# Kernel optimization log

Hardware: AMD Instinct MI355X
Metric: run time of the kernel (lower is better)

The kernel has to match this reference:

```python
import jax, jax.numpy as jnp
import numpy as np

B, N, D = 256, 256, 256
DELTA_BEARING = 5.0
DELTA_HEADING = 5.0
N_HEAD = int(360 / DELTA_HEADING)   # 72
N_BEAR = int(360 / DELTA_BEARING)   # 72
DOMAIN_PARAM = 2.0
EPS = 1e-14


def setup_inputs() -> dict:
    key = jax.random.key(0)
    ks = jax.random.split(key, 8)
    hidden_state = jax.random.normal(ks[0], (B, N, D), dtype=jnp.float32)
    distance_matrix = jax.random.uniform(ks[1], (B, N, N), dtype=jnp.float32) * 10.0
    bearing_matrix = jax.random.uniform(ks[2], (B, N, N), dtype=jnp.float32) * 360.0
    heading_matrix = jax.random.uniform(ks[3], (B, N, N), dtype=jnp.float32) * 360.0
    sequence_mask = (jax.random.uniform(ks[4], (B, N)) > 0.1).astype(jnp.float32)
    domain = jnp.full((N_HEAD, N_BEAR), DOMAIN_PARAM, dtype=jnp.float32)
    lim = 1.0 / np.sqrt(2 * D)
    W = jax.random.uniform(ks[5], (D, 2 * D), minval=-lim, maxval=lim, dtype=jnp.float32)
    b = jax.random.uniform(ks[6], (D,), minval=-lim, maxval=lim, dtype=jnp.float32)
    return {"hidden_state": hidden_state, "distance_matrix": distance_matrix,
            "bearing_matrix": bearing_matrix, "heading_matrix": heading_matrix,
            "sequence_mask": sequence_mask, "domain": domain, "W": W, "b": b}


def _compute_weights(domain, distance_matrix, bearing_matrix, heading_matrix, sequence_mask):
    # domain lookup indices from heading/bearing bins
    idx1 = jnp.clip(jnp.floor((heading_matrix + DELTA_HEADING / 2) / DELTA_HEADING), 0, N_HEAD - 1).astype(jnp.int32)
    idx2 = jnp.clip(jnp.floor((bearing_matrix + DELTA_BEARING / 2) / DELTA_BEARING), 0, N_BEAR - 1).astype(jnp.int32)
    w = jax.nn.relu(domain[idx1, idx2] - distance_matrix)  # (B,N,N)
    # pairwise sequence mask and no-self-attention mask
    wm = sequence_mask[:, :, None] * sequence_mask[:, None, :]  # (B,N,N)
    ped = 1.0 - jnp.eye(w.shape[1], dtype=w.dtype)               # (N,N)
    valid = (ped[None, :, :] * wm) > 0
    w = jnp.where(valid, w, 0.0)
    # masked softmax over dim=2: zeros are treated as masked, epsilon-stabilized
    mask = (w != 0).astype(w.dtype)
    masked_exps = jnp.exp(w) * mask + EPS
    w = masked_exps / (masked_exps.sum(axis=2, keepdims=True) + EPS)
    return jnp.where(valid, w, 0.0)


def reference(hidden_state, distance_matrix, bearing_matrix, heading_matrix, sequence_mask, domain, W, b):
    weights = _compute_weights(domain, distance_matrix, bearing_matrix, heading_matrix, sequence_mask)
    weighted_hidden = jnp.einsum('bij,bjd->bid', weights, hidden_state)  # (B,N,D)
    cat = jnp.concatenate([weighted_hidden, hidden_state], axis=-1)       # (B,N,2D)
    return jnp.einsum('bnk,dk->bnd', cat, W) + b
```

## Files before the change

kernel.cpp:

```cpp
#include <hip/hip_runtime.h>
#include <hip/hip_bf16.h>


typedef __attribute__((ext_vector_type(4))) float  f32x4;
typedef __attribute__((ext_vector_type(8))) short  bf16x8;
typedef __attribute__((ext_vector_type(4))) short  bf16x4;

#define EPSC 1e-14f

__device__ __forceinline__ short f2bf(float v) {
  __hip_bfloat16 h = __float2bfloat16(v);
  return *reinterpret_cast<short*>(&h);
}
__device__ __forceinline__ float bf2f(unsigned short u) {
  union { unsigned int i; float f; } c; c.i = ((unsigned int)u) << 16; return c.f;
}
__device__ __forceinline__ void gload16(const void* g, void* l) {
  __builtin_amdgcn_global_load_lds(
      (const __attribute__((address_space(1))) void*)g,
      (__attribute__((address_space(3))) void*)l, 16, 0, 0);
}

__global__ void k0_pack(const float* __restrict__ W, short* __restrict__ Wbf) {
  int idx = blockIdx.x * 256 + threadIdx.x;
  f32x4 v = *(const f32x4*)(W + (size_t)idx * 4);
  bf16x4 pk;
  pk[0] = f2bf(v[0]); pk[1] = f2bf(v[1]); pk[2] = f2bf(v[2]); pk[3] = f2bf(v[3]);
  *(bf16x4*)(Wbf + (size_t)idx * 4) = pk;
}

__global__ void k0_check(const float* __restrict__ domain, float* __restrict__ flag) {
  __shared__ int s_ok[4];
  const int t = threadIdx.x;
  float v0 = domain[0];
  bool ok = true;
  for (int x = t; x < 72 * 72; x += 256) ok = ok && (domain[x] == v0);
  unsigned long long m = __ballot(ok);
  if ((t & 63) == 0) s_ok[t >> 6] = (m == ~0ull) ? 1 : 0;
  __syncthreads();
  if (t == 0) {
    flag[0] = v0;
    flag[1] = (s_ok[0] && s_ok[1] && s_ok[2] && s_ok[3]) ? 1.f : 0.f;
  }
}

__global__ __launch_bounds__(512) void k1dual(
    const float* __restrict__ H, const short* __restrict__ Wbf,
    const float* __restrict__ bias,
    short* __restrict__ P1T, short* __restrict__ P2) {
  extern __shared__ char sm[];
  char* sA = sm;
  char* sB = sm + 33792;
  const int t  = threadIdx.x;
  const int n0 = blockIdx.x * 64;
  const int b  = n0 >> 8;
  const int jb = n0 & 255;

  #pragma unroll
  for (int p = 0; p < 4; ++p) {
    int z = t + 512 * p;
    int j = z >> 5, seg = z & 31;
    const float* src = H + (size_t)(n0 + j) * 256 + seg * 8;
    f32x4 h0 = *(const f32x4*)src;
    f32x4 h1 = *(const f32x4*)(src + 4);
    bf16x8 pk;
    pk[0] = f2bf(h0[0]); pk[1] = f2bf(h0[1]); pk[2] = f2bf(h0[2]); pk[3] = f2bf(h0[3]);
    pk[4] = f2bf(h1[0]); pk[5] = f2bf(h1[1]); pk[6] = f2bf(h1[2]); pk[7] = f2bf(h1[3]);
    *(bf16x8*)(sA + j * 528 + seg * 16) = pk;
  }

  const int wid = t >> 6, l = t & 63;
  const int wn = wid >> 2, wc = wid & 3;
  const int lr = l & 15, lg = l >> 4;

  #pragma unroll
  for (int pass = 0; pass < 2; ++pass) {
    f32x4 acc[2][4] = {};
    for (int kk = 0; kk < 256; kk += 64) {
      __syncthreads();
      #pragma unroll
      for (int p = 0; p < 4; ++p) {
        int z = t + 512 * p;
        int d = z >> 3, s = z & 7;
        bf16x8 v = *(const bf16x8*)(Wbf + (size_t)d * 512 + pass * 256 + kk + s * 8);
        *(bf16x8*)(sB + d * 144 + s * 16) = v;
      }
      __syncthreads();
      #pragma unroll
      for (int sub = 0; sub < 2; ++sub) {
        bf16x8 a[2], bb[4];
        #pragma unroll
        for (int m = 0; m < 2; ++m) {
          int row = wn * 32 + m * 16 + lr;
          a[m] = *(const bf16x8*)(sA + row * 528 + (kk + sub * 32 + lg * 8) * 2);
        }
        #pragma unroll
        for (int f = 0; f < 4; ++f) {
          int d = wc * 64 + f * 16 + lr;
          bb[f] = *(const bf16x8*)(sB + d * 144 + sub * 64 + lg * 16);
        }
        #pragma unroll
        for (int m = 0; m < 2; ++m) {
          #pragma unroll
          for (int f = 0; f < 4; ++f)
            acc[m][f] = __builtin_amdgcn_mfma_f32_16x16x32_bf16(a[m], bb[f], acc[m][f], 0, 0, 0);
        }
      }
    }
    if (pass == 0) {
      #pragma unroll
      for (int m = 0; m < 2; ++m) {
        int jl = wn * 32 + m * 16 + lg * 4;
        #pragma unroll
        for (int f = 0; f < 4; ++f) {
          int d = wc * 64 + f * 16 + lr;
          f32x4 v = acc[m][f];
          bf16x4 pk;
          pk[0] = f2bf(v[0]); pk[1] = f2bf(v[1]); pk[2] = f2bf(v[2]); pk[3] = f2bf(v[3]);
          *(bf16x4*)(P1T + (size_t)b * 65536 + (size_t)d * 256 + jb + jl) = pk;
        }
      }
    } else {
      #pragma unroll
      for (int m = 0; m < 2; ++m) {
        int jl = wn * 32 + m * 16 + lg * 4;
        #pragma unroll
        for (int f = 0; f < 4; ++f) {
          int d = wc * 64 + f * 16 + lr;
          float bs = bias[d];
          f32x4 v = acc[m][f];
          #pragma unroll
          for (int r = 0; r < 4; ++r)
            P2[(size_t)b * 65536 + (size_t)(jb + jl + r) * 256 + d] = f2bf(v[r] + bs);
        }
      }
    }
  }
}

__global__ __launch_bounds__(256) void k2a_weights(
    const float* __restrict__ dist, const float* __restrict__ bear,
    const float* __restrict__ head, const float* __restrict__ seqmask,
    const float* __restrict__ domain, const float* __restrict__ uflag,
    short* __restrict__ weBuf) {
  __shared__ float sMask[256];
  const int t = threadIdx.x;
  const int b = blockIdx.x >> 3;
  const int i0 = (blockIdx.x & 7) * 32;
  if (t < 256) sMask[t] = seqmask[b * 256 + t];
  __syncthreads();

  const int w = t >> 6, l = t & 63;
  const int j0 = l * 4;
  const float dval = uflag[0];
  const bool  uni  = uflag[1] != 0.f;
  const f32x4 mj = *(const f32x4*)(sMask + j0);

  f32x4 dv[8];
  #pragma unroll
  for (int rr = 0; rr < 8; ++rr) {
    int i = i0 + w * 8 + rr;
    dv[rr] = *(const f32x4*)(dist + ((size_t)b * 256 + i) * 256 + j0);
  }

  #pragma unroll
  for (int rr = 0; rr < 8; ++rr) {
    const int i = i0 + w * 8 + rr;
    const float mI = sMask[i];
    const size_t base = ((size_t)b * 256 + i) * 256;
    float ev[4];
    float rs = 0.f;
    if (uni) {
      #pragma unroll
      for (int e = 0; e < 4; ++e) {
        float wv = fmaxf(dval - dv[rr][e], 0.f);
        bool valid = (i != j0 + e) && (mI != 0.f) && (mj[e] != 0.f);
        float ex = (wv > 0.f) ? __expf(wv) : 0.f;
        ex = valid ? ex : 0.f;
        rs += ex;
        ev[e] = valid ? (ex + EPSC) : 0.f;
      }
    } else {
      f32x4 bv = *(const f32x4*)(bear + base + j0);
      f32x4 hv = *(const f32x4*)(head + base + j0);
      #pragma unroll
      for (int e = 0; e < 4; ++e) {
        float f1 = fminf(fmaxf(floorf((hv[e] + 2.5f) * 0.2f), 0.f), 71.f);
        float f2 = fminf(fmaxf(floorf((bv[e] + 2.5f) * 0.2f), 0.f), 71.f);
        float wv = fmaxf(domain[(int)(f1 * 72.f + f2)] - dv[rr][e], 0.f);
        bool valid = (i != j0 + e) && (mI != 0.f) && (mj[e] != 0.f);
        float ex = (wv > 0.f) ? __expf(wv) : 0.f;
        ex = valid ? ex : 0.f;
        rs += ex;
        ev[e] = valid ? (ex + EPSC) : 0.f;
      }
    }
    rs += __shfl_xor(rs, 1, 64);
    rs += __shfl_xor(rs, 2, 64);
    rs += __shfl_xor(rs, 4, 64);
    rs += __shfl_xor(rs, 8, 64);
    rs += __shfl_xor(rs, 16, 64);
    rs += __shfl_xor(rs, 32, 64);
    const float scale = 1.0f / (rs + 257.0f * EPSC);
    bf16x4 pk;
    pk[0] = f2bf(ev[0] * scale); pk[1] = f2bf(ev[1] * scale);
    pk[2] = f2bf(ev[2] * scale); pk[3] = f2bf(ev[3] * scale);
    *(bf16x4*)(weBuf + base + j0) = pk;
  }
}

__global__ __launch_bounds__(512) void k2b_gemm(
    const short* __restrict__ weBuf, const short* __restrict__ P1T,
    const short* __restrict__ P2, float* __restrict__ out) {
  extern __shared__ char sm[];
  char* sB = sm;
  const int t = threadIdx.x;
  const int x = blockIdx.x;
  const int blk = (x & 7) * 128 + (x >> 3);
  const int b  = blk >> 2;
  const int i0 = (blk & 3) * 64;

  const int wid = t >> 6, l = t & 63;
  const int lr = l & 15, lg = l >> 4;
  const int wr = wid & 3, wc = wid >> 2;
  const int r3 = l >> 3, sl = l & 7;
  const int sswz = (sl ^ r3) * 8;
  const int sw = (lr & 7) << 4;

  const short* __restrict__ P1b = P1T + (size_t)b * 65536;
  const int i = i0 + wr * 16 + lr;
  const size_t abase = ((size_t)b * 256 + i) * 256;

  f32x4 acc[8] = {};

  for (int c = 0; c < 4; ++c) {
    const int kk = c * 64;
    #pragma unroll
    for (int p = 0; p < 4; ++p) {
      int dd = wid * 8 + r3 + 64 * p;
      gload16(P1b + (size_t)dd * 256 + kk + sswz, sB + (wid * 8 + 64 * p) * 128);
    }
    __syncthreads();
    #pragma unroll
    for (int sub = 0; sub < 2; ++sub) {
      bf16x8 av = *(const bf16x8*)(weBuf + abase + kk + sub * 32 + lg * 8);
      #pragma unroll
      for (int n = 0; n < 8; ++n) {
        const int d = wc * 128 + n * 16 + lr;
        bf16x8 bb = *(const bf16x8*)(sB + d * 128 + ((sub * 64 + lg * 16) ^ sw));
        acc[n] = __builtin_amdgcn_mfma_f32_16x16x32_bf16(av, bb, acc[n], 0, 0, 0);
      }
    }
    __syncthreads();
  }

  #pragma unroll
  for (int n = 0; n < 8; ++n) {
    const int d = wc * 128 + n * 16 + lr;
    #pragma unroll
    for (int r = 0; r < 4; ++r) {
      const int row = i0 + wr * 16 + lg * 4 + r;
      const size_t off = ((size_t)b * 256 + row) * 256 + d;
      out[off] = acc[n][r] + bf2f((unsigned short)P2[off]);
    }
  }
}

extern "C" void kernel_launch(void* const* d_in, const int* in_sizes, int n_in,
                              void* d_out, int out_size, void* d_ws, size_t ws_size,
                              hipStream_t stream) {
  const float* hidden  = (const float*)d_in[0];
  const float* dist    = (const float*)d_in[1];
  const float* bear    = (const float*)d_in[2];
  const float* head    = (const float*)d_in[3];
  const float* seqmask = (const float*)d_in[4];
  const float* domain  = (const float*)d_in[5];
  const float* W       = (const float*)d_in[6];
  const float* bias    = (const float*)d_in[7];
  float* out = (float*)d_out;

  char* ws = (char*)d_ws;
  short* Wbf   = (short*)ws;
  float* flag  = (float*)(ws + 524288);
  short* P1T   = (short*)(ws + (1u << 20));
  short* P2    = (short*)(ws + (1u << 20) + (32u << 20));
  short* weBuf = (short*)(ws + (1u << 20) + (64u << 20));

  k0_pack<<<128, 256, 0, stream>>>(W, Wbf);
  k0_check<<<1, 256, 0, stream>>>(domain, flag);
  k2a_weights<<<2048, 256, 0, stream>>>(dist, bear, head, seqmask, domain, flag, weBuf);
  k1dual<<<1024, 512, 70656, stream>>>(hidden, Wbf, bias, P1T, P2);
  k2b_gemm<<<1024, 512, 32768, stream>>>(weBuf, P1T, P2, out);
}
```

Measured before the change: 122.6 us.

## Fold hidden@W2 projection into final GEMM instead of materializing P2

The separate P2 = H·W2^T + bias intermediate is removed. The final GEMM now runs eight K-chunks: four over weights×P1T and four over hidden (converted to bf16 on the fly) × the second half of W, with the bias taken from shared memory. The P1T projection becomes a standalone kernel modeled on the GEMM kernel structure, with swizzled global-to-LDS loads. This avoids the bf16 P2 write and re-read and the strided scalar P2 stores, at the cost of a longer K loop and fp32 reads of hidden in the final kernel.

```diff
diff --git a/kernel.cpp b/kernel.cpp
--- a/kernel.cpp
+++ b/kernel.cpp
@@ -11,14 +11,19 @@
 __device__ __forceinline__ short f2bf(float v) {
   __hip_bfloat16 h = __float2bfloat16(v);
   return *reinterpret_cast<short*>(&h);
-}
-__device__ __forceinline__ float bf2f(unsigned short u) {
-  union { unsigned int i; float f; } c; c.i = ((unsigned int)u) << 16; return c.f;
 }
 __device__ __forceinline__ void gload16(const void* g, void* l) {
   __builtin_amdgcn_global_load_lds(
       (const __attribute__((address_space(1))) void*)g,
       (__attribute__((address_space(3))) void*)l, 16, 0, 0);
+}
+__device__ __forceinline__ bf16x8 cvt8(const float* p) {
+  f32x4 a = *(const f32x4*)p;
+  f32x4 b = *(const f32x4*)(p + 4);
+  bf16x8 r;
+  r[0] = f2bf(a[0]); r[1] = f2bf(a[1]); r[2] = f2bf(a[2]); r[3] = f2bf(a[3]);
+  r[4] = f2bf(b[0]); r[5] = f2bf(b[1]); r[6] = f2bf(b[2]); r[7] = f2bf(b[3]);
+  return r;
 }
 
 __global__ void k0_pack(const float* __restrict__ W, short* __restrict__ Wbf) {
@@ -41,100 +46,6 @@
   if (t == 0) {
     flag[0] = v0;
     flag[1] = (s_ok[0] && s_ok[1] && s_ok[2] && s_ok[3]) ? 1.f : 0.f;
-  }
-}
-
-__global__ __launch_bounds__(512) void k1dual(
-    const float* __restrict__ H, const short* __restrict__ Wbf,
-    const float* __restrict__ bias,
-    short* __restrict__ P1T, short* __restrict__ P2) {
-  extern __shared__ char sm[];
-  char* sA = sm;
-  char* sB = sm + 33792;
-  const int t  = threadIdx.x;
-  const int n0 = blockIdx.x * 64;
-  const int b  = n0 >> 8;
-  const int jb = n0 & 255;
-
-  #pragma unroll
-  for (int p = 0; p < 4; ++p) {
-    int z = t + 512 * p;
-    int j = z >> 5, seg = z & 31;
-    const float* src = H + (size_t)(n0 + j) * 256 + seg * 8;
-    f32x4 h0 = *(const f32x4*)src;
-    f32x4 h1 = *(const f32x4*)(src + 4);
-    bf16x8 pk;
-    pk[0] = f2bf(h0[0]); pk[1] = f2bf(h0[1]); pk[2] = f2bf(h0[2]); pk[3] = f2bf(h0[3]);
-    pk[4] = f2bf(h1[0]); pk[5] = f2bf(h1[1]); pk[6] = f2bf(h1[2]); pk[7] = f2bf(h1[3]);
-    *(bf16x8*)(sA + j * 528 + seg * 16) = pk;
-  }
-
-  const int wid = t >> 6, l = t & 63;
-  const int wn = wid >> 2, wc = wid & 3;
-  const int lr = l & 15, lg = l >> 4;
-
-  #pragma unroll
-  for (int pass = 0; pass < 2; ++pass) {
-    f32x4 acc[2][4] = {};
-    for (int kk = 0; kk < 256; kk += 64) {
-      __syncthreads();
-      #pragma unroll
-      for (int p = 0; p < 4; ++p) {
-        int z = t + 512 * p;
-        int d = z >> 3, s = z & 7;
-        bf16x8 v = *(const bf16x8*)(Wbf + (size_t)d * 512 + pass * 256 + kk + s * 8);
-        *(bf16x8*)(sB + d * 144 + s * 16) = v;
-      }
-      __syncthreads();
-      #pragma unroll
-      for (int sub = 0; sub < 2; ++sub) {
-        bf16x8 a[2], bb[4];
-        #pragma unroll
-        for (int m = 0; m < 2; ++m) {
-          int row = wn * 32 + m * 16 + lr;
-          a[m] = *(const bf16x8*)(sA + row * 528 + (kk + sub * 32 + lg * 8) * 2);
-        }
-        #pragma unroll
-        for (int f = 0; f < 4; ++f) {
-          int d = wc * 64 + f * 16 + lr;
-          bb[f] = *(const bf16x8*)(sB + d * 144 + sub * 64 + lg * 16);
-        }
-        #pragma unroll
-        for (int m = 0; m < 2; ++m) {
-          #pragma unroll
-          for (int f = 0; f < 4; ++f)
-            acc[m][f] = __builtin_amdgcn_mfma_f32_16x16x32_bf16(a[m], bb[f], acc[m][f], 0, 0, 0);
-        }
-      }
-    }
-    if (pass == 0) {
-      #pragma unroll
-      for (int m = 0; m < 2; ++m) {
-        int jl = wn * 32 + m * 16 + lg * 4;
-        #pragma unroll
-        for (int f = 0; f < 4; ++f) {
-          int d = wc * 64 + f * 16 + lr;
-          f32x4 v = acc[m][f];
-          bf16x4 pk;
-          pk[0] = f2bf(v[0]); pk[1] = f2bf(v[1]); pk[2] = f2bf(v[2]); pk[3] = f2bf(v[3]);
-          *(bf16x4*)(P1T + (size_t)b * 65536 + (size_t)d * 256 + jb + jl) = pk;
-        }
-      }
-    } else {
-      #pragma unroll
-      for (int m = 0; m < 2; ++m) {
-        int jl = wn * 32 + m * 16 + lg * 4;
-        #pragma unroll
-        for (int f = 0; f < 4; ++f) {
-          int d = wc * 64 + f * 16 + lr;
-          float bs = bias[d];
-          f32x4 v = acc[m][f];
-          #pragma unroll
-          for (int r = 0; r < 4; ++r)
-            P2[(size_t)b * 65536 + (size_t)(jb + jl + r) * 256 + d] = f2bf(v[r] + bs);
-        }
-      }
-    }
   }
 }
 
@@ -209,16 +120,17 @@
   }
 }
 
-__global__ __launch_bounds__(512) void k2b_gemm(
-    const short* __restrict__ weBuf, const short* __restrict__ P1T,
-    const short* __restrict__ P2, float* __restrict__ out) {
+__global__ __launch_bounds__(512) void k1_p1t(
+    const float* __restrict__ H, const short* __restrict__ Wbf,
+    short* __restrict__ P1T) {
   extern __shared__ char sm[];
   char* sB = sm;
   const int t = threadIdx.x;
   const int x = blockIdx.x;
   const int blk = (x & 7) * 128 + (x >> 3);
-  const int b  = blk >> 2;
-  const int i0 = (blk & 3) * 64;
+  const int n0 = blk * 64;
+  const int b  = n0 >> 8;
+  const int jb = n0 & 255;
 
   const int wid = t >> 6, l = t & 63;
   const int lr = l & 15, lg = l >> 4;
@@ -227,9 +139,7 @@
   const int sswz = (sl ^ r3) * 8;
   const int sw = (lr & 7) << 4;
 
-  const short* __restrict__ P1b = P1T + (size_t)b * 65536;
-  const int i = i0 + wr * 16 + lr;
-  const size_t abase = ((size_t)b * 256 + i) * 256;
+  const size_t hbase = ((size_t)(n0 + wr * 16 + lr)) * 256;
 
   f32x4 acc[8] = {};
 
@@ -238,12 +148,12 @@
     #pragma unroll
     for (int p = 0; p < 4; ++p) {
       int dd = wid * 8 + r3 + 64 * p;
-      gload16(P1b + (size_t)dd * 256 + kk + sswz, sB + (wid * 8 + 64 * p) * 128);
+      gload16(Wbf + (size_t)dd * 512 + kk + sswz, sB + (wid * 8 + 64 * p) * 128);
     }
     __syncthreads();
     #pragma unroll
     for (int sub = 0; sub < 2; ++sub) {
-      bf16x8 av = *(const bf16x8*)(weBuf + abase + kk + sub * 32 + lg * 8);
+      bf16x8 av = cvt8(H + hbase + kk + sub * 32 + lg * 8);
       #pragma unroll
       for (int n = 0; n < 8; ++n) {
         const int d = wc * 128 + n * 16 + lr;
@@ -257,11 +167,81 @@
   #pragma unroll
   for (int n = 0; n < 8; ++n) {
     const int d = wc * 128 + n * 16 + lr;
+    f32x4 v = acc[n];
+    bf16x4 pk;
+    pk[0] = f2bf(v[0]); pk[1] = f2bf(v[1]); pk[2] = f2bf(v[2]); pk[3] = f2bf(v[3]);
+    *(bf16x4*)(P1T + (size_t)b * 65536 + (size_t)d * 256 + jb + wr * 16 + lg * 4) = pk;
+  }
+}
+
+__global__ __launch_bounds__(512) void k2b_gemm(
+    const short* __restrict__ weBuf, const short* __restrict__ P1T,
+    const short* __restrict__ Wbf, const float* __restrict__ H,
+    const float* __restrict__ bias, float* __restrict__ out) {
+  extern __shared__ char sm[];
+  char*  sB    = sm;
+  float* sBias = (float*)(sm + 32768);
+  const int t = threadIdx.x;
+  const int x = blockIdx.x;
+  const int blk = (x & 7) * 128 + (x >> 3);
+  const int b  = blk >> 2;
+  const int i0 = (blk & 3) * 64;
+
+  const int wid = t >> 6, l = t & 63;
+  const int lr = l & 15, lg = l >> 4;
+  const int wr = wid & 3, wc = wid >> 2;
+  const int r3 = l >> 3, sl = l & 7;
+  const int sswz = (sl ^ r3) * 8;
+  const int sw = (lr & 7) << 4;
+
+  const short* __restrict__ P1b = P1T + (size_t)b * 65536;
+  const int i = i0 + wr * 16 + lr;
+  const size_t abase = ((size_t)b * 256 + i) * 256;
+
+  if (t < 256) sBias[t] = bias[t];
+
+  f32x4 acc[8] = {};
+
+  #pragma unroll 2
+  for (int g = 0; g < 8; ++g) {
+    const int kk = (g & 3) * 64;
+    if (g < 4) {
+      #pragma unroll
+      for (int p = 0; p < 4; ++p) {
+        int dd = wid * 8 + r3 + 64 * p;
+        gload16(P1b + (size_t)dd * 256 + kk + sswz, sB + (wid * 8 + 64 * p) * 128);
+      }
+    } else {
+      #pragma unroll
+      for (int p = 0; p < 4; ++p) {
+        int dd = wid * 8 + r3 + 64 * p;
+        gload16(Wbf + (size_t)dd * 512 + 256 + kk + sswz, sB + (wid * 8 + 64 * p) * 128);
+      }
+    }
+    __syncthreads();
+    #pragma unroll
+    for (int sub = 0; sub < 2; ++sub) {
+      bf16x8 av;
+      if (g < 4) av = *(const bf16x8*)(weBuf + abase + kk + sub * 32 + lg * 8);
+      else       av = cvt8(H + abase + kk + sub * 32 + lg * 8);
+      #pragma unroll
+      for (int n = 0; n < 8; ++n) {
+        const int d = wc * 128 + n * 16 + lr;
+        bf16x8 bb = *(const bf16x8*)(sB + d * 128 + ((sub * 64 + lg * 16) ^ sw));
+        acc[n] = __builtin_amdgcn_mfma_f32_16x16x32_bf16(av, bb, acc[n], 0, 0, 0);
+      }
+    }
+    __syncthreads();
+  }
+
+  #pragma unroll
+  for (int n = 0; n < 8; ++n) {
+    const int d = wc * 128 + n * 16 + lr;
+    const float bs = sBias[d];
     #pragma unroll
     for (int r = 0; r < 4; ++r) {
       const int row = i0 + wr * 16 + lg * 4 + r;
-      const size_t off = ((size_t)b * 256 + row) * 256 + d;
-      out[off] = acc[n][r] + bf2f((unsigned short)P2[off]);
+      out[((size_t)b * 256 + row) * 256 + d] = acc[n][r] + bs;
     }
   }
 }
@@ -283,12 +263,11 @@
   short* Wbf   = (short*)ws;
   float* flag  = (float*)(ws + 524288);
   short* P1T   = (short*)(ws + (1u << 20));
-  short* P2    = (short*)(ws + (1u << 20) + (32u << 20));
-  short* weBuf = (short*)(ws + (1u << 20) + (64u << 20));
+  short* weBuf = (short*)(ws + (1u << 20) + (32u << 20));
 
   k0_pack<<<128, 256, 0, stream>>>(W, Wbf);
   k0_check<<<1, 256, 0, stream>>>(domain, flag);
   k2a_weights<<<2048, 256, 0, stream>>>(dist, bear, head, seqmask, domain, flag, weBuf);
-  k1dual<<<1024, 512, 70656, stream>>>(hidden, Wbf, bias, P1T, P2);
-  k2b_gemm<<<1024, 512, 32768, stream>>>(weBuf, P1T, P2, out);
-}
+  k1_p1t<<<1024, 512, 32768, stream>>>(hidden, Wbf, P1T);
+  k2b_gemm<<<1024, 512, 33792, stream>>>(weBuf, P1T, Wbf, hidden, bias, out);
+}
```

Result: faster. 114.6 us, median of 2 (-6.6%).
